# Kernel tuning notes

Measured on AMD Instinct MI355X. Metric: run time of the kernel, lower is better.

The kernel has to match this reference:

```python
import jax, jax.numpy as jnp
import numpy as np

BETA = 0.25  # commitment-loss weight from init


def setup_inputs() -> dict:
    key = jax.random.key(0)
    k1, k2 = jax.random.split(key)
    B, C, K, D = 8192, 4, 8192, 1024  # tokens, num_codebooks, codebook_size, codebook_dim
    x = jax.random.normal(k1, (B, C, D), dtype=jnp.float32)
    # nn.Embedding default init ~ N(0,1); scale like SimVQ (dim**-0.5) keeps values sane
    codebooks = jax.random.normal(k2, (C, K, D), dtype=jnp.float32) * (D ** -0.5)
    return {"x": x, "codebooks": codebooks}


def reference(x, codebooks):
    # x: [B, C, D]; codebooks: [C, K, D]
    B, C, D = x.shape
    K = codebooks.shape[1]
    sg = jax.lax.stop_gradient

    x2 = jnp.sum(x * x, axis=-1)[..., None]            # [B, C, 1]
    e2 = jnp.sum(codebooks * codebooks, axis=-1)       # [C, K]
    xe = jnp.einsum('bcd,ckd->bck', x, codebooks)      # [B, C, K]
    dist = x2 - 2.0 * xe + e2[None]                    # [B, C, K]

    embed_ind = jnp.argmin(dist, axis=-1)              # [B, C] int

    # gather quantized vectors: per-codebook embedding lookup
    x_q = codebooks[jnp.arange(C)[None, :], embed_ind]  # [B, C, D]

    # straight-through quantization losses, per codebook (mse over B*D), summed over codebooks
    l_codebook = jnp.mean((x_q - sg(x)) ** 2, axis=(0, 2))   # [C]
    l_commit = jnp.mean((x - sg(x_q)) ** 2, axis=(0, 2))     # [C]
    quant_loss = jnp.sum(l_codebook + BETA * l_commit)

    # unused code count per codebook (one-hot scatter-sum)
    counts = jnp.zeros((C, K), x.dtype).at[jnp.arange(C)[None, :], embed_ind].add(1.0)
    unused_codes = jnp.sum(counts == 0)

    x_q_st = x + sg(x_q - x)  # straight-through estimator
    return (x_q_st, quant_loss, unused_codes, embed_ind)
```

## Files before the change

kernel.cpp:

```cpp
#include <hip/hip_runtime.h>
#include <cstdio>
#include <cstdint>

typedef _Float16 f16;
typedef __attribute__((ext_vector_type(8))) _Float16 f16x8;
typedef __attribute__((ext_vector_type(4))) float f32x4;
typedef unsigned int u32;
typedef unsigned long long u64;

static constexpr int NB = 8192;
static constexpr int NC = 4;
static constexpr int NK = 8192;
static constexpr int ND = 1024;
static constexpr float SCALE_X = 1024.f;
static constexpr float SCALE_E = 4096.f;
static constexpr float RESCUE_THR = 3.5e-3f;
static constexpr float THR2 = 1.4e-4f;
static constexpr int MAXC  = 2048;
static constexpr int NSLOT = 128;
static constexpr int MAXF2 = 1024;
static constexpr int TPR   = 128;
static constexpr int CPT   = 64;
static constexpr int WSLOT = 8;

static constexpr long XQ_OFF = (long)NB * NC * ND;
static constexpr int G7BUF = 24576;
static constexpr int MBUF = 40960;

__device__ __forceinline__ void glds16(const void* g, void* l) {
  __builtin_amdgcn_global_load_lds((const __attribute__((address_space(1))) u32*)g,
                                   (__attribute__((address_space(3))) u32*)l, 16, 0, 0);
}

__device__ __forceinline__ bool lt2(float s, int i, float so, int io) {
  return s < so || (s == so && i < io);
}
__device__ __forceinline__ void merge_top2(float& s1, int& i1, float& s2, int& i2,
                                           float o1, int oi1, float o2, int oi2) {
  float a1, b1; int ai1, bi1;
  if (lt2(o1, oi1, s1, i1)) { a1 = o1; ai1 = oi1; b1 = s1; bi1 = i1; }
  else                      { a1 = s1; ai1 = i1;  b1 = o1; bi1 = oi1; }
  float c2 = s2; int ci2 = i2;
  if (lt2(o2, oi2, c2, ci2)) { c2 = o2; ci2 = oi2; }
  if (lt2(b1, bi1, c2, ci2)) { c2 = b1; ci2 = bi1; }
  s1 = a1; i1 = ai1; s2 = c2; i2 = ci2;
}
__device__ __forceinline__ bool lt2d(double s, int i, double so, int io) {
  return s < so || (s == so && i < io);
}
__device__ __forceinline__ void merge_top2d(double& s1, int& i1, double& s2, int& i2,
                                            double o1, int oi1, double o2, int oi2) {
  double a1, b1; int ai1, bi1;
  if (lt2d(o1, oi1, s1, i1)) { a1 = o1; ai1 = oi1; b1 = s1; bi1 = i1; }
  else                       { a1 = s1; ai1 = i1;  b1 = o1; bi1 = oi1; }
  double c2 = s2; int ci2 = i2;
  if (lt2d(o2, oi2, c2, ci2)) { c2 = o2; ci2 = oi2; }
  if (lt2d(b1, bi1, c2, ci2)) { c2 = b1; ci2 = bi1; }
  s1 = a1; i1 = ai1; s2 = c2; i2 = ci2;
}

__global__ __launch_bounds__(256) void prep_split(const float* __restrict__ src,
                                                  f16* __restrict__ hi, f16* __restrict__ lo,
                                                  int is_x) {
  int bid = blockIdx.x;
  int kt = bid & 31;
  int tile = (bid >> 5) & 63;
  int c = bid >> 11;
  int t = threadIdx.x;
  int row = t >> 1, h = t & 1;
  long srow = is_x ? ((long)(tile * 128 + row) * NC + c)
                   : ((long)c * NK + tile * 128 + row);
  const float* s = src + srow * ND + kt * 32 + h * 16;
  float sc = is_x ? SCALE_X : SCALE_E;
  float vbuf[16];
#pragma unroll
  for (int j = 0; j < 4; ++j) {
    float4 v = *(const float4*)(s + j * 4);
    vbuf[j*4+0]=v.x; vbuf[j*4+1]=v.y; vbuf[j*4+2]=v.z; vbuf[j*4+3]=v.w;
  }
  f16 hv[16], lv[16];
#pragma unroll
  for (int j = 0; j < 16; ++j) {
    float v = vbuf[j] * sc;
    f16 hh = (f16)v;
    hv[j] = hh;
    lv[j] = (f16)(v - (float)hh);
  }
  long tb = (long)bid * 4096;
#pragma unroll
  for (int kb = 0; kb < 2; ++kb) {
    long off = tb + (((long)(h*2 + kb) * 128 + row) << 3);
    f16x8 hx, lx;
#pragma unroll
    for (int e = 0; e < 8; ++e) { hx[e] = hv[kb*8+e]; lx[e] = lv[kb*8+e]; }
    *(f16x8*)(hi + off) = hx;
    *(f16x8*)(lo + off) = lx;
  }
}

__global__ __launch_bounds__(256) void prep1(const float* __restrict__ src,
                                             f16* __restrict__ hi, int is_x) {
  int bid = blockIdx.x;
  int kt = bid & 31;
  int tile = (bid >> 5) & 63;
  int c = bid >> 11;
  int t = threadIdx.x;
  int row = t >> 1, h = t & 1;
  long srow = is_x ? ((long)(tile * 128 + row) * NC + c)
                   : ((long)c * NK + tile * 128 + row);
  const float* s = src + srow * ND + kt * 32 + h * 16;
  float sc = is_x ? SCALE_X : SCALE_E;
  f16 hv[16];
#pragma unroll
  for (int j = 0; j < 4; ++j) {
    float4 v = *(const float4*)(s + j * 4);
    hv[j*4+0] = (f16)(v.x * sc); hv[j*4+1] = (f16)(v.y * sc);
    hv[j*4+2] = (f16)(v.z * sc); hv[j*4+3] = (f16)(v.w * sc);
  }
  long tb = (long)bid * 4096;
#pragma unroll
  for (int kb = 0; kb < 2; ++kb) {
    long off = tb + (((long)(h*2 + kb) * 128 + row) << 3);
    f16x8 hx;
#pragma unroll
    for (int e = 0; e < 8; ++e) hx[e] = hv[kb*8+e];
    *(f16x8*)(hi + off) = hx;
  }
}

__global__ __launch_bounds__(256) void row2_np(const float* __restrict__ src,
                                               float* __restrict__ dst) {
  int row = blockIdx.x * 32 + (threadIdx.x >> 3);
  int blk = threadIdx.x & 7;
  const float* p = src + (long)row * ND + blk * 128;
  float r[8];
  float4 a0 = *(const float4*)(p);
  float4 a1 = *(const float4*)(p + 4);
  r[0] = a0.x*a0.x; r[1] = a0.y*a0.y; r[2] = a0.z*a0.z; r[3] = a0.w*a0.w;
  r[4] = a1.x*a1.x; r[5] = a1.y*a1.y; r[6] = a1.z*a1.z; r[7] = a1.w*a1.w;
#pragma unroll
  for (int i = 1; i < 16; ++i) {
    float4 b0 = *(const float4*)(p + i * 8);
    float4 b1 = *(const float4*)(p + i * 8 + 4);
    r[0] += b0.x*b0.x; r[1] += b0.y*b0.y; r[2] += b0.z*b0.z; r[3] += b0.w*b0.w;
    r[4] += b1.x*b1.x; r[5] += b1.y*b1.y; r[6] += b1.z*b1.z; r[7] += b1.w*b1.w;
  }
  float res = ((r[0]+r[1])+(r[2]+r[3])) + ((r[4]+r[5])+(r[6]+r[7]));
  res += __shfl_xor(res, 1);
  res += __shfl_xor(res, 2);
  res += __shfl_xor(res, 4);
  if (blk == 0) dst[row] = res;
}

__global__ __launch_bounds__(256, 2) void vq_gemm7(
    const f16* __restrict__ xh, const f16* __restrict__ cbh,
    const float* __restrict__ e2np,
    u64* __restrict__ wsA, u64* __restrict__ wsB) {
  __shared__ char smem[3 * G7BUF + 8192];
  float* e2s = (float*)(smem + 3 * G7BUF);
  int bid0 = blockIdx.x;
  int bid = (bid0 & 7) * 64 + (bid0 >> 3);
  int nq = bid & 3;
  int mt = (bid >> 2) & 31;
  int c  = bid >> 7;
  int tid = threadIdx.x;
  int lane = tid & 63;
  int wid = tid >> 6;
  int g = lane >> 4, r16 = lane & 15;
  int wm = wid >> 1, wn = wid & 1;
  int n0 = wn * 64;
  int wub = (tid & 192) << 4;

  {
    const float4* src4 = (const float4*)(e2np + c * NK + nq * 2048);
    float4* dst4 = (float4*)e2s;
    for (int i = tid; i < 512; i += 256) dst4[i] = src4[i];
  }
  __syncthreads();

  auto stage = [&](int s, int bufi) {
    int ntl = s >> 5;
    int kt = s & 31;
    char* sb = smem + bufi * G7BUF;
#pragma unroll
    for (int tb = 0; tb < 2; ++tb) {
      long ca = ((long)(c * 64 + mt * 2 + tb) * 32 + kt) * 4096;
#pragma unroll
      for (int part = 0; part < 2; ++part)
        glds16((const char*)(xh + ca) + part * 4096 + tid * 16,
               sb + tb * 8192 + part * 4096 + wub);
    }
    long cbk = ((long)(c * 64 + nq * 16 + ntl) * 32 + kt) * 4096;
#pragma unroll
    for (int part = 0; part < 2; ++part)
      glds16((const char*)(cbh + cbk) + part * 4096 + tid * 16,
             sb + 16384 + part * 4096 + wub);
  };

  f32x4 acc[8][4];
#pragma unroll
  for (int i = 0; i < 8; ++i)
#pragma unroll
    for (int j = 0; j < 4; ++j) acc[i][j] = f32x4{0.f, 0.f, 0.f, 0.f};

  float run_s[2], run_s2[2];
  int run_i[2], run_i2[2];
#pragma unroll
  for (int j = 0; j < 2; ++j) {
    run_s[j] = 1e30f; run_s2[j] = 1e30f;
    run_i[j] = 0x7fffffff; run_i2[j] = 0x7fffffff;
  }

  stage(0, 0);
  stage(1, 1);

  const int TSTEPS = 512;
#pragma unroll 1
  for (int t = 0; t < TSTEPS; ++t) {
    if (t < TSTEPS - 1) { asm volatile("s_waitcnt vmcnt(6)" ::: "memory"); }
    else                { asm volatile("s_waitcnt vmcnt(0)" ::: "memory"); }
    __builtin_amdgcn_s_barrier();
    __builtin_amdgcn_sched_barrier(0);

    const char* sb    = smem + (t % 3) * G7BUF;
    const char* baseA = sb + wm * 8192;
    const char* baseB = sb + 16384;
    int bi2 = (t + 2) % 3;
    bool pf = (t + 2 < TSTEPS);

    f16x8 fb[4];
#pragma unroll
    for (int nf = 0; nf < 4; ++nf)
      fb[nf] = *(const f16x8*)(baseB + ((g * 128 + n0 + nf * 16 + r16) << 4));
    f16x8 fa[8];
#pragma unroll
    for (int mf = 0; mf < 8; ++mf)
      fa[mf] = *(const f16x8*)(baseA + ((g * 128 + mf * 16 + r16) << 4));
    if (pf) stage(t + 2, bi2);
    __builtin_amdgcn_s_setprio(1);
#pragma unroll
    for (int mf = 0; mf < 8; ++mf)
#pragma unroll
      for (int nf = 0; nf < 4; ++nf)
        acc[mf][nf] = __builtin_amdgcn_mfma_f32_16x16x32_f16(fa[mf], fb[nf], acc[mf][nf], 0, 0, 0);
    __builtin_amdgcn_s_setprio(0);

    if ((t & 31) == 31) {
      int ntl = t >> 5;
      float he2[4]; int col[4];
#pragma unroll
      for (int nf = 0; nf < 4; ++nf) {
        int lc = ntl * 128 + n0 + nf * 16 + r16;
        col[nf] = nq * 2048 + lc;
        he2[nf] = 0.5f * e2s[lc];
      }
#pragma unroll
      for (int mf = 0; mf < 8; ++mf)
#pragma unroll
        for (int q = 0; q < 4; ++q) {
          float s1 = __fmaf_rn(acc[mf][0][q], -0x1p-22f, he2[0]);
          int i1 = col[0];
          float s2 = 1e30f; int i2 = 0x7fffffff;
#pragma unroll
          for (int nf = 1; nf < 4; ++nf) {
            float sv = __fmaf_rn(acc[mf][nf][q], -0x1p-22f, he2[nf]);
            int ci = col[nf];
            if (lt2(sv, ci, s1, i1)) { s2 = s1; i2 = i1; s1 = sv; i1 = ci; }
            else if (lt2(sv, ci, s2, i2)) { s2 = sv; i2 = ci; }
          }
#pragma unroll
          for (int w = 1; w < 16; w <<= 1) {
            float o1 = __shfl_xor(s1, w);
            int  oi1 = __shfl_xor(i1, w);
            float o2 = __shfl_xor(s2, w);
            int  oi2 = __shfl_xor(i2, w);
            merge_top2(s1, i1, s2, i2, o1, oi1, o2, oi2);
          }
          if (((mf * 4 + q) & 15) == r16) {
            constexpr_j:;
            const int j = (mf * 4 + q) >> 4;
            merge_top2(run_s[j], run_i[j], run_s2[j], run_i2[j], s1, i1, s2, i2);
          }
        }
#pragma unroll
      for (int mf = 0; mf < 8; ++mf)
#pragma unroll
        for (int nf = 0; nf < 4; ++nf)
          acc[mf][nf] = f32x4{0.f, 0.f, 0.f, 0.f};
    }
  }

#pragma unroll
  for (int j = 0; j < 2; ++j) {
    int slotid = j * 16 + r16;
    int mf = slotid >> 2, q = slotid & 3;
    int brow = mt * 256 + wm * 128 + mf * 16 + g * 4 + q;
    long idx = ((long)brow * NC + c) * WSLOT + (nq * 2 + wn);
    wsA[idx] = ((u64)__float_as_uint(run_s[j])  << 32) | (u32)run_i[j];
    wsB[idx] = ((u64)__float_as_uint(run_s2[j]) << 32) | (u32)run_i2[j];
  }
}

__global__ __launch_bounds__(256) void flag_collect2(
    const u64* __restrict__ wsA, const u64* __restrict__ wsB,
    int* __restrict__ fidx, int* __restrict__ flagc, int* __restrict__ nfc) {
  int row = blockIdx.x * 256 + threadIdx.x;
  if (row >= NB * NC) return;
  float g1 = 1e30f, g2 = 1e30f; int gi1 = 0x7fffffff, gi2 = 0x7fffffff;
  for (int s = 0; s < WSLOT; ++s) {
    u64 a = wsA[(long)row * WSLOT + s];
    u64 b = wsB[(long)row * WSLOT + s];
    merge_top2(g1, gi1, g2, gi2,
               __uint_as_float((u32)(a >> 32)), (int)(u32)(a & 0xffffffffu),
               __uint_as_float((u32)(b >> 32)), (int)(u32)(b & 0xffffffffu));
  }
  int c = row & (NC - 1);
  if (__fsub_rn(g2, g1) < RESCUE_THR) {
    int idx = atomicAdd(&nfc[c], 1);
    if (idx < MAXC) flagc[c * MAXC + idx] = row;
    else fidx[row] = gi1;
  } else {
    fidx[row] = gi1;
  }
}

__global__ __launch_bounds__(256) void gather_split(
    const float* __restrict__ x, const int* __restrict__ flagc,
    const int* __restrict__ nfc, f16* __restrict__ mxh, f16* __restrict__ mxl) {
  int bid = blockIdx.x;
  int kt = bid & 31;
  int ft = (bid >> 5) & 31;
  int c = bid >> 10;
  int nR = nfc[c]; if (nR > MAXC) nR = MAXC;
  if (ft * 64 >= nR) return;
  int t = threadIdx.x;
  int row = t >> 2, seg = t & 3;
  int fi = ft * 64 + row;
  int srow = flagc[c * MAXC + (fi < nR ? fi : nR - 1)];
  const float* s = x + (long)srow * ND + kt * 32 + seg * 8;
  float vbuf[8];
  float4 v0 = *(const float4*)(s);
  float4 v1 = *(const float4*)(s + 4);
  vbuf[0]=v0.x; vbuf[1]=v0.y; vbuf[2]=v0.z; vbuf[3]=v0.w;
  vbuf[4]=v1.x; vbuf[5]=v1.y; vbuf[6]=v1.z; vbuf[7]=v1.w;
  f16x8 hx, lx;
#pragma unroll
  for (int j = 0; j < 8; ++j) {
    float v = vbuf[j] * SCALE_X;
    f16 hh = (f16)v;
    hx[j] = hh;
    lx[j] = (f16)(v - (float)hh);
  }
  long off = ((long)((c * 32 + ft) * 32 + kt)) * 2048 + ((seg * 64 + row) << 3);
  *(f16x8*)(mxh + off) = hx;
  *(f16x8*)(mxl + off) = lx;
}

__global__ __launch_bounds__(256, 2) void mini_gemm(
    const f16* __restrict__ mxh, const f16* __restrict__ mxl,
    const f16* __restrict__ cbh, const f16* __restrict__ cbl,
    const float* __restrict__ e2np, const int* __restrict__ nfc,
    u64* __restrict__ msA, u64* __restrict__ msB) {
  __shared__ char smem[2 * MBUF];
  int bid = blockIdx.x;
  int ct = bid & 31;
  int ft = (bid >> 5) & 31;
  int c = bid >> 10;
  int nR = nfc[c]; if (nR > MAXC) nR = MAXC;
  if (ft * 64 >= nR) return;
  int tid = threadIdx.x;
  int lane = tid & 63;
  int wn = tid >> 6;
  int g = lane >> 4, r16 = lane & 15;
  int ntl = wn >> 1;
  int cb0 = (wn & 1) * 64;
  int wub = (tid & 192) << 4;

  auto stage = [&](int kt, int bufi) {
    char* sb = smem + bufi * MBUF;
    long ca = ((long)((c * 32 + ft) * 32 + kt)) * 2048;
    glds16((const char*)(mxh + ca) + tid * 16, sb + wub);
    glds16((const char*)(mxl + ca) + tid * 16, sb + 4096 + wub);
#pragma unroll
    for (int nl = 0; nl < 2; ++nl) {
      long cbk = ((long)(c * 64 + ct * 2 + nl) * 32 + kt) * 4096;
#pragma unroll
      for (int half = 0; half < 2; ++half) {
        glds16((const char*)(cbh + cbk) + half * 4096 + tid * 16,
               sb + 8192 + nl * 8192 + half * 4096 + wub);
        glds16((const char*)(cbl + cbk) + half * 4096 + tid * 16,
               sb + 24576 + nl * 8192 + half * 4096 + wub);
      }
    }
  };

  f32x4 acc[4][4];
#pragma unroll
  for (int i = 0; i < 4; ++i)
#pragma unroll
    for (int j = 0; j < 4; ++j) acc[i][j] = f32x4{0.f, 0.f, 0.f, 0.f};

  stage(0, 0);
#pragma unroll 1
  for (int t = 0; t < 32; ++t) {
    __syncthreads();
    if (t + 1 < 32) stage(t + 1, (t + 1) & 1);
    const char* base = smem + (t & 1) * MBUF;
    const char* bBh = base + 8192 + ntl * 8192;
    const char* bBl = base + 24576 + ntl * 8192;
    f16x8 fah[4], fal[4], fbh[4], fbl[4];
#pragma unroll
    for (int mf = 0; mf < 4; ++mf) {
      int off = (g * 64 + mf * 16 + r16) << 4;
      fah[mf] = *(const f16x8*)(base + off);
      fal[mf] = *(const f16x8*)(base + 4096 + off);
    }
#pragma unroll
    for (int nf = 0; nf < 4; ++nf) {
      int off = (g * 128 + cb0 + nf * 16 + r16) << 4;
      fbh[nf] = *(const f16x8*)(bBh + off);
      fbl[nf] = *(const f16x8*)(bBl + off);
    }
#pragma unroll
    for (int mf = 0; mf < 4; ++mf)
#pragma unroll
      for (int nf = 0; nf < 4; ++nf) {
        acc[mf][nf] = __builtin_amdgcn_mfma_f32_16x16x32_f16(fah[mf], fbh[nf], acc[mf][nf], 0, 0, 0);
        acc[mf][nf] = __builtin_amdgcn_mfma_f32_16x16x32_f16(fah[mf], fbl[nf], acc[mf][nf], 0, 0, 0);
        acc[mf][nf] = __builtin_amdgcn_mfma_f32_16x16x32_f16(fal[mf], fbh[nf], acc[mf][nf], 0, 0, 0);
      }
  }

  float he2[4]; int col[4];
#pragma unroll
  for (int nf = 0; nf < 4; ++nf) {
    col[nf] = ct * 256 + wn * 64 + nf * 16 + r16;
    he2[nf] = 0.5f * e2np[c * NK + col[nf]];
  }
#pragma unroll
  for (int mf = 0; mf < 4; ++mf)
#pragma unroll
    for (int q = 0; q < 4; ++q) {
      float s1 = __fmaf_rn(acc[mf][0][q], -0x1p-22f, he2[0]);
      int i1 = col[0];
      float s2 = 1e30f; int i2 = 0x7fffffff;
#pragma unroll
      for (int nf = 1; nf < 4; ++nf) {
        float sv = __fmaf_rn(acc[mf][nf][q], -0x1p-22f, he2[nf]);
        int ci = col[nf];
        if (lt2(sv, ci, s1, i1)) { s2 = s1; i2 = i1; s1 = sv; i1 = ci; }
        else if (lt2(sv, ci, s2, i2)) { s2 = sv; i2 = ci; }
      }
#pragma unroll
      for (int w = 1; w < 16; w <<= 1) {
        float o1 = __shfl_xor(s1, w);
        int  oi1 = __shfl_xor(i1, w);
        float o2 = __shfl_xor(s2, w);
        int  oi2 = __shfl_xor(i2, w);
        merge_top2(s1, i1, s2, i2, o1, oi1, o2, oi2);
      }
      if (r16 == 0) {
        int fi = ft * 64 + mf * 16 + g * 4 + q;
        int slot = ct * 4 + wn;
        long idx = ((long)(c * MAXC + fi)) * NSLOT + slot;
        msA[idx] = ((u64)__float_as_uint(s1) << 32) | (u32)i1;
        msB[idx] = ((u64)__float_as_uint(s2) << 32) | (u32)i2;
      }
    }
}

__global__ __launch_bounds__(256) void mini_flag(
    const int* __restrict__ flagc, const int* __restrict__ nfc,
    const u64* __restrict__ msA, const u64* __restrict__ msB,
    int* __restrict__ fidx, int* __restrict__ flag2, int* __restrict__ nf2) {
  int c = blockIdx.x >> 9;
  int fi = (blockIdx.x & 511) * 4 + (threadIdx.x >> 6);
  int nR = nfc[c]; if (nR > MAXC) nR = MAXC;
  if (fi >= nR) return;
  int lane = threadIdx.x & 63;
  long base = ((long)(c * MAXC + fi)) * NSLOT;
  u64 a0 = msA[base + lane],      b0 = msB[base + lane];
  u64 a1 = msA[base + lane + 64], b1 = msB[base + lane + 64];
  float s1 = __uint_as_float((u32)(a0 >> 32));
  int   i1 = (int)(u32)(a0 & 0xffffffffu);
  float s2 = __uint_as_float((u32)(b0 >> 32));
  int   i2 = (int)(u32)(b0 & 0xffffffffu);
  merge_top2(s1, i1, s2, i2,
             __uint_as_float((u32)(a1 >> 32)), (int)(u32)(a1 & 0xffffffffu),
             __uint_as_float((u32)(b1 >> 32)), (int)(u32)(b1 & 0xffffffffu));
#pragma unroll
  for (int w = 1; w < 64; w <<= 1) {
    float o1 = __shfl_xor(s1, w);
    int  oi1 = __shfl_xor(i1, w);
    float o2 = __shfl_xor(s2, w);
    int  oi2 = __shfl_xor(i2, w);
    merge_top2(s1, i1, s2, i2, o1, oi1, o2, oi2);
  }
  if (lane == 0) {
    int row = flagc[c * MAXC + fi];
    if (__fsub_rn(s2, s1) < THR2) {
      int idx = atomicAdd(nf2, 1);
      if (idx < MAXF2) flag2[idx] = row;
      else fidx[row] = i1;
    } else {
      fidx[row] = i1;
    }
  }
}

__global__ __launch_bounds__(256) void rescue_scan(
    const float* __restrict__ x, const float* __restrict__ cb,
    const int* __restrict__ flaglist, const int* __restrict__ nflag,
    double* __restrict__ pb1, double* __restrict__ pb2,
    int* __restrict__ pk1, int* __restrict__ pk2) {
  int nf = *nflag; if (nf > MAXF2) nf = MAXF2;
  int ntask = nf * TPR;
  int wv = blockIdx.x * 4 + (threadIdx.x >> 6);
  int lane = threadIdx.x & 63;
  for (int task = wv; task < ntask; task += 4096) {
    int fi = task >> 7, ch = task & (TPR - 1);
    int row = flaglist[fi];
    int c = row & (NC - 1);
    const float* xr = x + (long)row * ND + lane * 4;
    float4 xv0 = *(const float4*)(xr);
    float4 xv1 = *(const float4*)(xr + 256);
    float4 xv2 = *(const float4*)(xr + 512);
    float4 xv3 = *(const float4*)(xr + 768);
    double b1 = 1e300, b2 = 1e300; int k1 = 0x7fffffff, k2 = 0x7fffffff;
    const float* eb = cb + ((long)c * NK + ch * CPT) * ND + lane * 4;
    for (int kk = 0; kk < CPT; ++kk) {
      const float* e = eb + (long)kk * ND;
      float4 e0 = *(const float4*)(e);
      float4 e1 = *(const float4*)(e + 256);
      float4 e2v = *(const float4*)(e + 512);
      float4 e3 = *(const float4*)(e + 768);
      double d = 0.0;
      double f;
      f = (double)xv0.x - (double)e0.x;  d = fma(f, f, d);
      f = (double)xv0.y - (double)e0.y;  d = fma(f, f, d);
      f = (double)xv0.z - (double)e0.z;  d = fma(f, f, d);
      f = (double)xv0.w - (double)e0.w;  d = fma(f, f, d);
      f = (double)xv1.x - (double)e1.x;  d = fma(f, f, d);
      f = (double)xv1.y - (double)e1.y;  d = fma(f, f, d);
      f = (double)xv1.z - (double)e1.z;  d = fma(f, f, d);
      f = (double)xv1.w - (double)e1.w;  d = fma(f, f, d);
      f = (double)xv2.x - (double)e2v.x; d = fma(f, f, d);
      f = (double)xv2.y - (double)e2v.y; d = fma(f, f, d);
      f = (double)xv2.z - (double)e2v.z; d = fma(f, f, d);
      f = (double)xv2.w - (double)e2v.w; d = fma(f, f, d);
      f = (double)xv3.x - (double)e3.x;  d = fma(f, f, d);
      f = (double)xv3.y - (double)e3.y;  d = fma(f, f, d);
      f = (double)xv3.z - (double)e3.z;  d = fma(f, f, d);
      f = (double)xv3.w - (double)e3.w;  d = fma(f, f, d);
#pragma unroll
      for (int w = 1; w < 64; w <<= 1) d += __shfl_xor(d, w);
      int k = ch * CPT + kk;
      if (lt2d(d, k, b1, k1)) { b2 = b1; k2 = k1; b1 = d; k1 = k; }
      else if (lt2d(d, k, b2, k2)) { b2 = d; k2 = k; }
    }
    if (lane == 0) { pb1[task] = b1; pb2[task] = b2; pk1[task] = k1; pk2[task] = k2; }
  }
}

__global__ __launch_bounds__(256) void rescue_verdict(
    const float* __restrict__ x, const float* __restrict__ cb,
    const int* __restrict__ flaglist, const int* __restrict__ nflag,
    const double* __restrict__ pb1, const double* __restrict__ pb2,
    const int* __restrict__ pk1, const int* __restrict__ pk2,
    int* __restrict__ fidx) {
  int nf = *nflag; if (nf > MAXF2) nf = MAXF2;
  int fi = blockIdx.x;
  if (fi >= nf) return;
  int row = flaglist[fi];
  int c = row & (NC - 1);
  int t = threadIdx.x;
  __shared__ float xs[ND];
  __shared__ int sAB[2];
  __shared__ double sh_xe[2], sh_e2[2], sh_x2;
  for (int i = t; i < ND; i += 256) xs[i] = x[(long)row * ND + i];
  if (t == 0) {
    double m1 = 1e300, m2 = 1e300; int a1 = 0x7fffffff, a2 = 0x7fffffff;
    for (int p = 0; p < TPR; ++p) {
      long pi = (long)fi * TPR + p;
      merge_top2d(m1, a1, m2, a2, pb1[pi], pk1[pi], pb2[pi], pk2[pi]);
    }
    sAB[0] = a1; sAB[1] = a2;
  }
  __syncthreads();
  int A = sAB[0], B = sAB[1];
  int lane = t & 63, wvv = t >> 6;
  if (wvv < 2) {
    const float* e = cb + ((long)c * NK + (wvv ? B : A)) * ND;
    double xe = 0, e2 = 0;
    for (int j = lane; j < ND; j += 64) {
      double ev = (double)e[j], xv = (double)xs[j];
      xe = fma(xv, ev, xe);
      e2 = fma(ev, ev, e2);
    }
    for (int w = 1; w < 64; w <<= 1) { xe += __shfl_xor(xe, w); e2 += __shfl_xor(e2, w); }
    if (lane == 0) { sh_xe[wvv] = xe; sh_e2[wvv] = e2; }
  } else if (wvv == 2) {
    double x2 = 0;
    for (int j = lane; j < ND; j += 64) { double xv = (double)xs[j]; x2 = fma(xv, xv, x2); }
    for (int w = 1; w < 64; w <<= 1) x2 += __shfl_xor(x2, w);
    if (lane == 0) sh_x2 = x2;
  }
  __syncthreads();
  if (t == 0) {
    float x2f = (float)sh_x2;
    float e2A = (float)sh_e2[0], e2B = (float)sh_e2[1];
    double xeA = sh_xe[0], xeB = sh_xe[1];
    const double JX = 3.0e-6;
    int cntA = 0, cntB = 0;
    for (int u = -3; u <= 3; ++u) {
      float x2c = __uint_as_float((u32)((int)__float_as_uint(x2f) + u));
      for (int j = 0; j < 4; ++j) {
        double jit = (j == 2) ? JX : (j == 3) ? -JX : 0.0;
        float xeAf = (float)(xeA + jit);
        float xeBf = (float)(xeB - jit);
        float DA = __fadd_rn(__fsub_rn(x2c, __fmul_rn(2.0f, xeAf)), e2A);
        float DB = __fadd_rn(__fsub_rn(x2c, __fmul_rn(2.0f, xeBf)), e2B);
        bool pickA = (DA < DB) || (DA == DB && A < B);
        if (pickA) ++cntA; else ++cntB;
      }
    }
    int pick = (cntA > cntB) ? A : (cntB > cntA) ? B : (A < B ? A : B);
    fidx[row] = pick;
  }
}

__global__ __launch_bounds__(256) void gather_kernel(
    const float* __restrict__ x, const float* __restrict__ cb,
    const int* __restrict__ fidx, float* __restrict__ out,
    int* __restrict__ counts, double* __restrict__ loss) {
  int bid = blockIdx.x;
  int c = bid & (NC - 1);
  int t = threadIdx.x;
  int k = fidx[bid];
  const float* e  = cb + ((long)c * NK + k) * ND + t * 4;
  const float* xv = x + (long)bid * ND + t * 4;
  float* dst = out + (long)bid * ND + t * 4;
  float4 ev = *(const float4*)e;
  float4 x4 = *(const float4*)xv;
  float d0 = ev.x - x4.x, d1 = ev.y - x4.y, d2 = ev.z - x4.z, d3 = ev.w - x4.w;
  float4 o; o.x = x4.x + d0; o.y = x4.y + d1; o.z = x4.z + d2; o.w = x4.w + d3;
  *(float4*)dst = o;
  float ls = d0*d0 + d1*d1 + d2*d2 + d3*d3;
#pragma unroll
  for (int w = 1; w < 64; w <<= 1) ls += __shfl_xor(ls, w);
  __shared__ float part[4];
  if ((t & 63) == 0) part[t >> 6] = ls;
  __syncthreads();
  if (t == 0) {
    double tot = (double)part[0] + (double)part[1] + (double)part[2] + (double)part[3];
    atomicAdd(&loss[c], tot);
    out[XQ_OFF + 2 + bid] = (float)k;
    atomicAdd(&counts[c * NK + k], 1);
  }
}

__global__ __launch_bounds__(256) void finalize_kernel(const int* __restrict__ counts,
                                                       const double* __restrict__ loss,
                                                       float* __restrict__ out) {
  int t = threadIdx.x;
  int cnt = 0;
  for (int i = t; i < NC * NK; i += 256) cnt += (counts[i] == 0) ? 1 : 0;
#pragma unroll
  for (int w = 1; w < 64; w <<= 1) cnt += __shfl_xor(cnt, w);
  __shared__ int part[4];
  if ((t & 63) == 0) part[t >> 6] = cnt;
  __syncthreads();
  if (t == 0) {
    int total = part[0] + part[1] + part[2] + part[3];
    double s = loss[0] + loss[1] + loss[2] + loss[3];
    out[XQ_OFF + 0] = (float)(1.25 * s / (double)((long)NB * ND));
    out[XQ_OFF + 1] = (float)total;
  }
}

extern "C" void kernel_launch(void* const* d_in, const int* in_sizes, int n_in,
                              void* d_out, int out_size, void* d_ws, size_t ws_size,
                              hipStream_t stream) {
  (void)in_sizes; (void)n_in; (void)out_size;
  const float* x  = (const float*)d_in[0];
  const float* cb = (const float*)d_in[1];
  float* out = (float*)d_out;
  char* ws = (char*)d_ws;

  size_t sz_half = (size_t)NC * NK * ND * sizeof(f16);
  size_t sz_mini = (size_t)NC * MAXC * ND * sizeof(f16);
  size_t off = 0;
  f16* cbh = (f16*)(ws + off); off += sz_half;
  f16* cbl = (f16*)(ws + off); off += sz_half;
  f16* xh  = (f16*)(ws + off); off += sz_half;
  f16* mxh = (f16*)(ws + off); off += sz_mini;
  f16* mxl = (f16*)(ws + off); off += sz_mini;
  float* e2np = (float*)(ws + off); off += (size_t)NC * NK * 4;
  u64*  wsA   = (u64*)(ws + off);   off += (size_t)NB * NC * WSLOT * 8;
  u64*  wsB   = (u64*)(ws + off);   off += (size_t)NB * NC * WSLOT * 8;
  u64*  msA   = (u64*)(ws + off);   off += (size_t)NC * MAXC * NSLOT * 8;
  u64*  msB   = (u64*)(ws + off);   off += (size_t)NC * MAXC * NSLOT * 8;
  int*  fidx  = (int*)(ws + off);   off += (size_t)NB * NC * 4;
  int*  counts= (int*)(ws + off);   off += (size_t)NC * NK * 4;
  double* loss= (double*)(ws + off);off += 256;
  int*  nfc   = (int*)(ws + off);   off += 256;
  int*  flagc = (int*)(ws + off);   off += (size_t)NC * MAXC * 4;
  int*  nf2   = (int*)(ws + off);   off += 256;
  int*  flag2 = (int*)(ws + off);   off += (size_t)MAXF2 * 4;
  double* pb1 = (double*)(ws + off);off += (size_t)MAXF2 * TPR * 8;
  double* pb2 = (double*)(ws + off);off += (size_t)MAXF2 * TPR * 8;
  int*  pk1   = (int*)(ws + off);   off += (size_t)MAXF2 * TPR * 4;
  int*  pk2   = (int*)(ws + off);   off += (size_t)MAXF2 * TPR * 4;
  if (ws_size < off) {
    fprintf(stderr, "kernel_launch: workspace too small: need %zu, have %zu\n", off, ws_size);
    return;
  }

  hipMemsetAsync(counts, 0, (size_t)NC * NK * 4, stream);
  hipMemsetAsync(loss, 0, 256, stream);
  hipMemsetAsync(nfc, 0, 256, stream);
  hipMemsetAsync(nf2, 0, 256, stream);

  prep_split<<<NC * 64 * 32, 256, 0, stream>>>(cb, cbh, cbl, 0);
  prep1<<<NC * 64 * 32, 256, 0, stream>>>(x, xh, 1);
  row2_np<<<(NC * NK) / 32, 256, 0, stream>>>(cb, e2np);
  vq_gemm7<<<NC * 32 * 4, 256, 0, stream>>>(xh, cbh, e2np, wsA, wsB);

  flag_collect2<<<(NB * NC) / 256, 256, 0, stream>>>(wsA, wsB, fidx, flagc, nfc);
  gather_split<<<NC * 32 * 32, 256, 0, stream>>>(x, flagc, nfc, mxh, mxl);
  mini_gemm<<<NC * 32 * 32, 256, 0, stream>>>(mxh, mxl, cbh, cbl, e2np, nfc, msA, msB);
  mini_flag<<<NC * 512, 256, 0, stream>>>(flagc, nfc, msA, msB, fidx, flag2, nf2);
  rescue_scan<<<1024, 256, 0, stream>>>(x, cb, flag2, nf2, pb1, pb2, pk1, pk2);
  rescue_verdict<<<MAXF2, 256, 0, stream>>>(x, cb, flag2, nf2, pb1, pb2, pk1, pk2, fidx);

  gather_kernel<<<NB * NC, 256, 0, stream>>>(x, cb, fidx, out, counts, loss);
  finalize_kernel<<<1, 256, 0, stream>>>(counts, loss, out);
}
```

Before: 1.653 ms.

## Enlarge distance GEMM tile to 256x256 with 8 waves and double-buffered K-chunks

The main distance GEMM now runs as 256 blocks of 512 threads (8 waves) instead of 512 blocks of 256 threads. Each block covers 256 rows by 256 codebook columns per N-tile, which halves the A-tile reloads per output. The pipeline also changes from a 3-buffer ring with one stage per step to a 2-buffer scheme, where each step splits into four phases that interleave A and B loads with the MFMAs. This should raise arithmetic intensity and cut redundant global and LDS traffic. In exchange it uses about 144KB of LDS at one block per CU and has fewer blocks to cover the 256 CUs.

Result: no change. 1.675 ms (+1.3%).

```diff
diff --git a/kernel.cpp b/kernel.cpp
--- a/kernel.cpp
+++ b/kernel.cpp
@@ -24,7 +24,7 @@
 static constexpr int WSLOT = 8;
 
 static constexpr long XQ_OFF = (long)NB * NC * ND;
-static constexpr int G7BUF = 24576;
+static constexpr int BUFK = 65536;
 static constexpr int MBUF = 40960;
 
 __device__ __forceinline__ void glds16(const void* g, void* l) {
@@ -152,49 +152,78 @@
   if (blk == 0) dst[row] = res;
 }
 
-__global__ __launch_bounds__(256, 2) void vq_gemm7(
+#define GPHASE(MFH, KK, GATE, ISSUE)                                              \
+  {                                                                               \
+    if (GATE) { asm volatile("s_waitcnt vmcnt(4)" ::: "memory"); }                \
+    __builtin_amdgcn_s_barrier();                                                 \
+    __builtin_amdgcn_sched_barrier(0);                                            \
+    const char* bufA = smem + (T & 1) * BUFK + (KK) * 16384 + wmb;                \
+    const char* bufB = smem + (T & 1) * BUFK + 32768 + (KK) * 16384 + ctb;        \
+    f16x8 fa[4], fb[4];                                                           \
+    _Pragma("unroll")                                                             \
+    for (int i = 0; i < 4; ++i)                                                   \
+      fa[i] = *(const f16x8*)(bufA + ((g * 128 + ((MFH) * 4 + i) * 16 + r16) << 4)); \
+    _Pragma("unroll")                                                             \
+    for (int nf = 0; nf < 4; ++nf)                                                \
+      fb[nf] = *(const f16x8*)(bufB + ((g * 128 + nb0 + nf * 16 + r16) << 4));    \
+    ISSUE;                                                                        \
+    __builtin_amdgcn_s_setprio(1);                                                \
+    _Pragma("unroll")                                                             \
+    for (int i = 0; i < 4; ++i) {                                                 \
+      _Pragma("unroll")                                                           \
+      for (int nf = 0; nf < 4; ++nf)                                              \
+        acc[(MFH) * 4 + i][nf] = __builtin_amdgcn_mfma_f32_16x16x32_f16(          \
+            fa[i], fb[nf], acc[(MFH) * 4 + i][nf], 0, 0, 0);                      \
+    }                                                                             \
+    __builtin_amdgcn_s_setprio(0);                                                \
+  }
+
+__global__ __launch_bounds__(512, 1) void vq_gemm8(
     const f16* __restrict__ xh, const f16* __restrict__ cbh,
     const float* __restrict__ e2np,
     u64* __restrict__ wsA, u64* __restrict__ wsB) {
-  __shared__ char smem[3 * G7BUF + 8192];
-  float* e2s = (float*)(smem + 3 * G7BUF);
+  __shared__ char smem[2 * BUFK + 16384];
+  float* e2s = (float*)(smem + 2 * BUFK);
   int bid0 = blockIdx.x;
-  int bid = (bid0 & 7) * 64 + (bid0 >> 3);
-  int nq = bid & 3;
-  int mt = (bid >> 2) & 31;
-  int c  = bid >> 7;
+  int bid = (bid0 & 7) * 32 + (bid0 >> 3);
+  int nh = bid & 1;
+  int mt = (bid >> 1) & 31;
+  int c  = bid >> 6;
   int tid = threadIdx.x;
   int lane = tid & 63;
   int wid = tid >> 6;
   int g = lane >> 4, r16 = lane & 15;
-  int wm = wid >> 1, wn = wid & 1;
-  int n0 = wn * 64;
-  int wub = (tid & 192) << 4;
+  int wm = wid >> 2, wn = wid & 3;
+  int wmb = wm * 8192;
+  int ctb = (wn >> 1) * 8192;
+  int nb0 = (wn & 1) * 64;
+  int wub = (tid & 448) << 4;
 
   {
-    const float4* src4 = (const float4*)(e2np + c * NK + nq * 2048);
+    const float4* src4 = (const float4*)(e2np + c * NK + nh * 4096);
     float4* dst4 = (float4*)e2s;
-    for (int i = tid; i < 512; i += 256) dst4[i] = src4[i];
+    for (int i = tid; i < 1024; i += 512) dst4[i] = src4[i];
   }
   __syncthreads();
 
-  auto stage = [&](int s, int bufi) {
-    int ntl = s >> 5;
-    int kt = s & 31;
-    char* sb = smem + bufi * G7BUF;
-#pragma unroll
-    for (int tb = 0; tb < 2; ++tb) {
-      long ca = ((long)(c * 64 + mt * 2 + tb) * 32 + kt) * 4096;
-#pragma unroll
-      for (int part = 0; part < 2; ++part)
-        glds16((const char*)(xh + ca) + part * 4096 + tid * 16,
-               sb + tb * 8192 + part * 4096 + wub);
-    }
-    long cbk = ((long)(c * 64 + nq * 16 + ntl) * 32 + kt) * 4096;
-#pragma unroll
-    for (int part = 0; part < 2; ++part)
-      glds16((const char*)(cbh + cbk) + part * 4096 + tid * 16,
-             sb + 16384 + part * 4096 + wub);
+  auto stageA = [&](int Tn, int kk) {
+    int kt = ((Tn & 15) << 1) + kk;
+    char* dst = smem + (Tn & 1) * BUFK + kk * 16384;
+#pragma unroll
+    for (int rt = 0; rt < 2; ++rt) {
+      long el = ((long)(c * 64 + mt * 2 + rt) * 32 + kt) * 4096;
+      glds16((const char*)(xh + el) + tid * 16, dst + rt * 8192 + wub);
+    }
+  };
+  auto stageB = [&](int Tn, int kk) {
+    int ntl = Tn >> 4;
+    int kt = ((Tn & 15) << 1) + kk;
+    char* dst = smem + (Tn & 1) * BUFK + 32768 + kk * 16384;
+#pragma unroll
+    for (int ct = 0; ct < 2; ++ct) {
+      long el = ((long)(c * 64 + nh * 32 + ntl * 2 + ct) * 32 + kt) * 4096;
+      glds16((const char*)(cbh + el) + tid * 16, dst + ct * 8192 + wub);
+    }
   };
 
   f32x4 acc[8][4];
@@ -211,47 +240,24 @@
     run_i[j] = 0x7fffffff; run_i2[j] = 0x7fffffff;
   }
 
-  stage(0, 0);
-  stage(1, 1);
-
-  const int TSTEPS = 512;
+  stageA(0, 0); stageB(0, 0); stageA(0, 1); stageB(0, 1);
+
+  const int NTK = 256;
 #pragma unroll 1
-  for (int t = 0; t < TSTEPS; ++t) {
-    if (t < TSTEPS - 1) { asm volatile("s_waitcnt vmcnt(6)" ::: "memory"); }
-    else                { asm volatile("s_waitcnt vmcnt(0)" ::: "memory"); }
-    __builtin_amdgcn_s_barrier();
-    __builtin_amdgcn_sched_barrier(0);
-
-    const char* sb    = smem + (t % 3) * G7BUF;
-    const char* baseA = sb + wm * 8192;
-    const char* baseB = sb + 16384;
-    int bi2 = (t + 2) % 3;
-    bool pf = (t + 2 < TSTEPS);
-
-    f16x8 fb[4];
-#pragma unroll
-    for (int nf = 0; nf < 4; ++nf)
-      fb[nf] = *(const f16x8*)(baseB + ((g * 128 + n0 + nf * 16 + r16) << 4));
-    f16x8 fa[8];
-#pragma unroll
-    for (int mf = 0; mf < 8; ++mf)
-      fa[mf] = *(const f16x8*)(baseA + ((g * 128 + mf * 16 + r16) << 4));
-    if (pf) stage(t + 2, bi2);
-    __builtin_amdgcn_s_setprio(1);
-#pragma unroll
-    for (int mf = 0; mf < 8; ++mf)
-#pragma unroll
-      for (int nf = 0; nf < 4; ++nf)
-        acc[mf][nf] = __builtin_amdgcn_mfma_f32_16x16x32_f16(fa[mf], fb[nf], acc[mf][nf], 0, 0, 0);
-    __builtin_amdgcn_s_setprio(0);
-
-    if ((t & 31) == 31) {
-      int ntl = t >> 5;
+  for (int T = 0; T < NTK; ++T) {
+    bool more = (T + 1 < NTK);
+    GPHASE(0, 0, true,  if (more) stageA(T + 1, 0));
+    GPHASE(1, 0, false, if (more) stageB(T + 1, 0));
+    GPHASE(0, 1, true,  if (more) stageA(T + 1, 1));
+    GPHASE(1, 1, false, if (more) stageB(T + 1, 1));
+
+    if ((T & 15) == 15) {
+      int ntl = T >> 4;
       float he2[4]; int col[4];
 #pragma unroll
       for (int nf = 0; nf < 4; ++nf) {
-        int lc = ntl * 128 + n0 + nf * 16 + r16;
-        col[nf] = nq * 2048 + lc;
+        int lc = ntl * 256 + wn * 64 + nf * 16 + r16;
+        col[nf] = nh * 4096 + lc;
         he2[nf] = 0.5f * e2s[lc];
       }
 #pragma unroll
@@ -277,7 +283,6 @@
             merge_top2(s1, i1, s2, i2, o1, oi1, o2, oi2);
           }
           if (((mf * 4 + q) & 15) == r16) {
-            constexpr_j:;
             const int j = (mf * 4 + q) >> 4;
             merge_top2(run_s[j], run_i[j], run_s2[j], run_i2[j], s1, i1, s2, i2);
           }
@@ -295,7 +300,7 @@
     int slotid = j * 16 + r16;
     int mf = slotid >> 2, q = slotid & 3;
     int brow = mt * 256 + wm * 128 + mf * 16 + g * 4 + q;
-    long idx = ((long)brow * NC + c) * WSLOT + (nq * 2 + wn);
+    long idx = ((long)brow * NC + c) * WSLOT + (nh * 4 + wn);
     wsA[idx] = ((u64)__float_as_uint(run_s[j])  << 32) | (u32)run_i[j];
     wsB[idx] = ((u64)__float_as_uint(run_s2[j]) << 32) | (u32)run_i2[j];
   }
@@ -724,7 +729,7 @@
   prep_split<<<NC * 64 * 32, 256, 0, stream>>>(cb, cbh, cbl, 0);
   prep1<<<NC * 64 * 32, 256, 0, stream>>>(x, xh, 1);
   row2_np<<<(NC * NK) / 32, 256, 0, stream>>>(cb, e2np);
-  vq_gemm7<<<NC * 32 * 4, 256, 0, stream>>>(xh, cbh, e2np, wsA, wsB);
+  vq_gemm8<<<NC * 32 * 2, 512, 0, stream>>>(xh, cbh, e2np, wsA, wsB);
 
   flag_collect2<<<(NB * NC) / 256, 256, 0, stream>>>(wsA, wsB, fidx, flagc, nfc);
   gather_split<<<NC * 32 * 32, 256, 0, stream>>>(x, flagc, nfc, mxh, mxl);
```

## Shrink main GEMM tile to 128x128 with double buffering for higher occupancy

Applied to the files above, without the earlier changes.

Replaces the 256x128-tile, triple-buffered distance GEMM with a 128x128 tile, double-buffered version that targets 5 blocks per CU. Each block covers 1024 codes instead of 2048, so partial top-2 slots per row double and the grid grows fourfold. The e2 norms are read straight from global memory instead of being staged in LDS, and three small memsets are merged into one by making the counters contiguous. The aim is to hide latency through occupancy rather than deep prefetch, at the cost of less operand reuse per block, more global traffic and a full vmcnt(0) wait on every step.

Result: slower. 3.321 ms (+100.9%).

```diff
diff --git a/kernel.cpp b/kernel.cpp
--- a/kernel.cpp
+++ b/kernel.cpp
@@ -21,10 +21,10 @@
 static constexpr int MAXF2 = 1024;
 static constexpr int TPR   = 128;
 static constexpr int CPT   = 64;
-static constexpr int WSLOT = 8;
+static constexpr int WSLOT = 16;
 
 static constexpr long XQ_OFF = (long)NB * NC * ND;
-static constexpr int G7BUF = 24576;
+static constexpr int GBUF10 = 16384;
 static constexpr int MBUF = 40960;
 
 __device__ __forceinline__ void glds16(const void* g, void* l) {
@@ -152,94 +152,72 @@
   if (blk == 0) dst[row] = res;
 }
 
-__global__ __launch_bounds__(256, 2) void vq_gemm7(
+__global__ __launch_bounds__(256, 5) void vq_gemm10(
     const f16* __restrict__ xh, const f16* __restrict__ cbh,
     const float* __restrict__ e2np,
     u64* __restrict__ wsA, u64* __restrict__ wsB) {
-  __shared__ char smem[3 * G7BUF + 8192];
-  float* e2s = (float*)(smem + 3 * G7BUF);
+  __shared__ char smem[2 * GBUF10];
   int bid0 = blockIdx.x;
-  int bid = (bid0 & 7) * 64 + (bid0 >> 3);
-  int nq = bid & 3;
-  int mt = (bid >> 2) & 31;
-  int c  = bid >> 7;
+  int bid = (bid0 & 7) * 256 + (bid0 >> 3);
+  int ng = bid & 7;
+  int mt = (bid >> 3) & 63;
+  int c  = bid >> 9;
   int tid = threadIdx.x;
   int lane = tid & 63;
   int wid = tid >> 6;
   int g = lane >> 4, r16 = lane & 15;
   int wm = wid >> 1, wn = wid & 1;
-  int n0 = wn * 64;
+  int m0 = wm * 64, n0 = wn * 64;
   int wub = (tid & 192) << 4;
-
-  {
-    const float4* src4 = (const float4*)(e2np + c * NK + nq * 2048);
-    float4* dst4 = (float4*)e2s;
-    for (int i = tid; i < 512; i += 256) dst4[i] = src4[i];
-  }
-  __syncthreads();
 
   auto stage = [&](int s, int bufi) {
     int ntl = s >> 5;
     int kt = s & 31;
-    char* sb = smem + bufi * G7BUF;
-#pragma unroll
-    for (int tb = 0; tb < 2; ++tb) {
-      long ca = ((long)(c * 64 + mt * 2 + tb) * 32 + kt) * 4096;
-#pragma unroll
-      for (int part = 0; part < 2; ++part)
-        glds16((const char*)(xh + ca) + part * 4096 + tid * 16,
-               sb + tb * 8192 + part * 4096 + wub);
-    }
-    long cbk = ((long)(c * 64 + nq * 16 + ntl) * 32 + kt) * 4096;
-#pragma unroll
-    for (int part = 0; part < 2; ++part)
+    char* sb = smem + bufi * GBUF10;
+    long ca = ((long)(c * 64 + mt) * 32 + kt) * 4096;
+    long cbk = ((long)(c * 64 + ng * 8 + ntl) * 32 + kt) * 4096;
+#pragma unroll
+    for (int part = 0; part < 2; ++part) {
+      glds16((const char*)(xh + ca) + part * 4096 + tid * 16,
+             sb + part * 4096 + wub);
       glds16((const char*)(cbh + cbk) + part * 4096 + tid * 16,
-             sb + 16384 + part * 4096 + wub);
+             sb + 8192 + part * 4096 + wub);
+    }
   };
 
-  f32x4 acc[8][4];
-#pragma unroll
-  for (int i = 0; i < 8; ++i)
+  f32x4 acc[4][4];
+#pragma unroll
+  for (int i = 0; i < 4; ++i)
 #pragma unroll
     for (int j = 0; j < 4; ++j) acc[i][j] = f32x4{0.f, 0.f, 0.f, 0.f};
 
-  float run_s[2], run_s2[2];
-  int run_i[2], run_i2[2];
-#pragma unroll
-  for (int j = 0; j < 2; ++j) {
-    run_s[j] = 1e30f; run_s2[j] = 1e30f;
-    run_i[j] = 0x7fffffff; run_i2[j] = 0x7fffffff;
-  }
+  float run_s = 1e30f, run_s2 = 1e30f;
+  int run_i = 0x7fffffff, run_i2 = 0x7fffffff;
 
   stage(0, 0);
-  stage(1, 1);
-
-  const int TSTEPS = 512;
+
+  const int TSTEPS = 256;
 #pragma unroll 1
   for (int t = 0; t < TSTEPS; ++t) {
-    if (t < TSTEPS - 1) { asm volatile("s_waitcnt vmcnt(6)" ::: "memory"); }
-    else                { asm volatile("s_waitcnt vmcnt(0)" ::: "memory"); }
+    asm volatile("s_waitcnt vmcnt(0)" ::: "memory");
     __builtin_amdgcn_s_barrier();
     __builtin_amdgcn_sched_barrier(0);
 
-    const char* sb    = smem + (t % 3) * G7BUF;
-    const char* baseA = sb + wm * 8192;
-    const char* baseB = sb + 16384;
-    int bi2 = (t + 2) % 3;
-    bool pf = (t + 2 < TSTEPS);
-
-    f16x8 fb[4];
+    const char* base  = smem + (t & 1) * GBUF10;
+    const char* baseB = base + 8192;
+    bool pf = (t + 1 < TSTEPS);
+
+    f16x8 fb[4], fa[4];
 #pragma unroll
     for (int nf = 0; nf < 4; ++nf)
       fb[nf] = *(const f16x8*)(baseB + ((g * 128 + n0 + nf * 16 + r16) << 4));
-    f16x8 fa[8];
-#pragma unroll
-    for (int mf = 0; mf < 8; ++mf)
-      fa[mf] = *(const f16x8*)(baseA + ((g * 128 + mf * 16 + r16) << 4));
-    if (pf) stage(t + 2, bi2);
+#pragma unroll
+    for (int mf = 0; mf < 4; ++mf)
+      fa[mf] = *(const f16x8*)(base + ((g * 128 + m0 + mf * 16 + r16) << 4));
+    if (pf) stage(t + 1, (t + 1) & 1);
     __builtin_amdgcn_s_setprio(1);
 #pragma unroll
-    for (int mf = 0; mf < 8; ++mf)
+    for (int mf = 0; mf < 4; ++mf)
 #pragma unroll
       for (int nf = 0; nf < 4; ++nf)
         acc[mf][nf] = __builtin_amdgcn_mfma_f32_16x16x32_f16(fa[mf], fb[nf], acc[mf][nf], 0, 0, 0);
@@ -250,12 +228,11 @@
       float he2[4]; int col[4];
 #pragma unroll
       for (int nf = 0; nf < 4; ++nf) {
-        int lc = ntl * 128 + n0 + nf * 16 + r16;
-        col[nf] = nq * 2048 + lc;
-        he2[nf] = 0.5f * e2s[lc];
+        col[nf] = ng * 1024 + ntl * 128 + n0 + nf * 16 + r16;
+        he2[nf] = 0.5f * e2np[c * NK + col[nf]];
       }
 #pragma unroll
-      for (int mf = 0; mf < 8; ++mf)
+      for (int mf = 0; mf < 4; ++mf)
 #pragma unroll
         for (int q = 0; q < 4; ++q) {
           float s1 = __fmaf_rn(acc[mf][0][q], -0x1p-22f, he2[0]);
@@ -276,28 +253,23 @@
             int  oi2 = __shfl_xor(i2, w);
             merge_top2(s1, i1, s2, i2, o1, oi1, o2, oi2);
           }
-          if (((mf * 4 + q) & 15) == r16) {
-            constexpr_j:;
-            const int j = (mf * 4 + q) >> 4;
-            merge_top2(run_s[j], run_i[j], run_s2[j], run_i2[j], s1, i1, s2, i2);
-          }
+          if (mf * 4 + q == r16)
+            merge_top2(run_s, run_i, run_s2, run_i2, s1, i1, s2, i2);
         }
 #pragma unroll
-      for (int mf = 0; mf < 8; ++mf)
+      for (int mf = 0; mf < 4; ++mf)
 #pragma unroll
         for (int nf = 0; nf < 4; ++nf)
           acc[mf][nf] = f32x4{0.f, 0.f, 0.f, 0.f};
     }
   }
 
-#pragma unroll
-  for (int j = 0; j < 2; ++j) {
-    int slotid = j * 16 + r16;
-    int mf = slotid >> 2, q = slotid & 3;
-    int brow = mt * 256 + wm * 128 + mf * 16 + g * 4 + q;
-    long idx = ((long)brow * NC + c) * WSLOT + (nq * 2 + wn);
-    wsA[idx] = ((u64)__float_as_uint(run_s[j])  << 32) | (u32)run_i[j];
-    wsB[idx] = ((u64)__float_as_uint(run_s2[j]) << 32) | (u32)run_i2[j];
+  {
+    int mf = r16 >> 2, q = r16 & 3;
+    int brow = mt * 128 + m0 + mf * 16 + g * 4 + q;
+    long idx = ((long)brow * NC + c) * WSLOT + (ng * 2 + wn);
+    wsA[idx] = ((u64)__float_as_uint(run_s)  << 32) | (u32)run_i;
+    wsB[idx] = ((u64)__float_as_uint(run_s2) << 32) | (u32)run_i2;
   }
 }
 
@@ -704,8 +676,8 @@
   int*  counts= (int*)(ws + off);   off += (size_t)NC * NK * 4;
   double* loss= (double*)(ws + off);off += 256;
   int*  nfc   = (int*)(ws + off);   off += 256;
+  int*  nf2   = (int*)(ws + off);   off += 256;
   int*  flagc = (int*)(ws + off);   off += (size_t)NC * MAXC * 4;
-  int*  nf2   = (int*)(ws + off);   off += 256;
   int*  flag2 = (int*)(ws + off);   off += (size_t)MAXF2 * 4;
   double* pb1 = (double*)(ws + off);off += (size_t)MAXF2 * TPR * 8;
   double* pb2 = (double*)(ws + off);off += (size_t)MAXF2 * TPR * 8;
@@ -717,14 +689,12 @@
   }
 
   hipMemsetAsync(counts, 0, (size_t)NC * NK * 4, stream);
-  hipMemsetAsync(loss, 0, 256, stream);
-  hipMemsetAsync(nfc, 0, 256, stream);
-  hipMemsetAsync(nf2, 0, 256, stream);
+  hipMemsetAsync(loss, 0, 768, stream);
 
   prep_split<<<NC * 64 * 32, 256, 0, stream>>>(cb, cbh, cbl, 0);
   prep1<<<NC * 64 * 32, 256, 0, stream>>>(x, xh, 1);
   row2_np<<<(NC * NK) / 32, 256, 0, stream>>>(cb, e2np);
-  vq_gemm7<<<NC * 32 * 4, 256, 0, stream>>>(xh, cbh, e2np, wsA, wsB);
+  vq_gemm10<<<NC * 64 * 8, 256, 0, stream>>>(xh, cbh, e2np, wsA, wsB);
 
   flag_collect2<<<(NB * NC) / 256, 256, 0, stream>>>(wsA, wsB, fidx, flagc, nfc);
   gather_split<<<NC * 32 * 32, 256, 0, stream>>>(x, flagc, nfc, mxh, mxl);
```
